# Optimization experiments

Hardware: AMD Instinct MI355X
Metric: run time of the kernel (lower is better)

## Reference

```python
import jax, jax.numpy as jnp
import numpy as np

A_CUBIC = -0.75  # torch grid_sample bicubic convolution coefficient
INTERP_FACTOR = 0.25
WINDOW = 20
STEP = 4


def _cubic_interp_1d(signal):
    # Replicates torch bicubic grid_sample (align_corners=True, border padding)
    # on a (B,1,1,n) tensor, which reduces to 1D cubic convolution (A=-0.75).
    B, n = signal.shape
    num_points = int((n - 1) / INTERP_FACTOR) + 1
    pos = jnp.linspace(0.0, n - 1, num_points)  # sample positions in index space
    i0 = jnp.floor(pos).astype(jnp.int32)
    s = (pos - i0).astype(signal.dtype)  # frac in [0,1)
    A = A_CUBIC
    def w_far(d):   # 1 <= d <= 2
        return ((A * d - 5 * A) * d + 8 * A) * d - 4 * A
    def w_near(d):  # 0 <= d <= 1
        return ((A + 2) * d - (A + 3)) * d * d + 1
    w = jnp.stack([w_far(s + 1), w_near(s), w_near(1 - s), w_far(2 - s)], axis=-1)  # (P,4)
    idx = jnp.clip(i0[:, None] + jnp.arange(-1, 3)[None, :], 0, n - 1)  # border pad, (P,4)
    vals = signal[:, idx]  # (B,P,4)
    return jnp.einsum('bpk,pk->bp', vals, w)


def _apply_kernels(x, gamma_raw):
    # per-row shift so min >= 0 (only if min < 0), then softmax-weighted kernel mix
    m = jnp.min(x, axis=1, keepdims=True)
    x = x - jnp.minimum(m, 0.0)
    gamma = jax.nn.softmax(gamma_raw)
    poly = (x + 1.3) ** 2                      # polynomial: degree=2, offset=1.3
    gauss = jnp.exp(-0.5 * (x - 0.7) ** 2)     # gaussian: center=0.7, sigma=1.0
    return gamma[0] * poly + gamma[1] * gauss


def setup_inputs() -> dict:
    key = jax.random.key(0)
    return {
        'signal': jax.random.normal(key, (4, 1000), dtype=jnp.float32),
        'alpha': jnp.float32(0.15),
        'beta': jnp.float32(0.9),
        'gamma_raw': jnp.array([0.5, 0.5], dtype=jnp.float32),
    }


def reference(signal, alpha, beta, gamma_raw):
    interp = _cubic_interp_1d(signal)              # (B, n)
    ks = _apply_kernels(interp, gamma_raw)         # (B, n)
    B, n = ks.shape
    n_windows = (n - WINDOW) // STEP + 1
    starts = jnp.arange(n_windows) * STEP          # (W,)
    posn = jnp.arange(n)                           # (n,)
    in_win = (posn[None, :] >= starts[:, None]) & (posn[None, :] < starts[:, None] + WINDOW)
    in_win = in_win.astype(ks.dtype)               # (W, n)
    sig = ks[:, None, :]                           # (B,1,n)
    # M: fft of zero-padded window; M1: fft of signal with window zeroed out
    M = jnp.abs(jnp.fft.fft(sig * in_win[None], axis=-1))          # (B,W,n)
    M1 = jnp.abs(jnp.fft.fft(sig * (1.0 - in_win)[None], axis=-1))  # (B,W,n)
    x_max = jnp.max(M, axis=-1, keepdims=True)
    strong = (M > x_max * alpha).astype(M.dtype)
    combined = M1 * M * strong
    result = jnp.minimum(M, combined)              # (B,W,n)
    thr = beta * jnp.max(result.reshape(B, -1), axis=1)[:, None, None]
    result = result * (result > thr).astype(result.dtype)
    return result
```

## Files before the change

### kernel.cpp

```cpp
#include <hip/hip_runtime.h>
#include <math.h>

#define NSIG 1000
#define NP   3997
#define KHALF 1999
#define NW   995
#define WIN  20
#define STEPW 4
#define BATCH 4
#define NCH  125
#define CW   8


__device__ __forceinline__ double interp_at(const float* __restrict__ s, int p) {
    int i0 = p >> 2;
    int si = p & 3;
    double ss = 0.25 * (double)si;
    const double A = -0.75;
    double d0 = ss + 1.0;
    double w0 = ((A * d0 - 5.0 * A) * d0 + 8.0 * A) * d0 - 4.0 * A;
    double w1 = ((A + 2.0) * ss - (A + 3.0)) * ss * ss + 1.0;
    double d2 = 1.0 - ss;
    double w2 = ((A + 2.0) * d2 - (A + 3.0)) * d2 * d2 + 1.0;
    double d3 = 2.0 - ss;
    double w3 = ((A * d3 - 5.0 * A) * d3 + 8.0 * A) * d3 - 4.0 * A;
    int im1 = i0 - 1; if (im1 < 0) im1 = 0;
    int ip1 = i0 + 1; if (ip1 > NSIG - 1) ip1 = NSIG - 1;
    int ip2 = i0 + 2; if (ip2 > NSIG - 1) ip2 = NSIG - 1;
    return w0 * (double)s[im1] + w1 * (double)s[i0] +
           w2 * (double)s[ip1] + w3 * (double)s[ip2];
}

__global__ __launch_bounds__(512) void dft_init_kernel(
        const float* __restrict__ sig, const float* __restrict__ gamma_raw,
        float* __restrict__ ks, float2* __restrict__ tw, float2* __restrict__ S,
        unsigned int* __restrict__ rmax) {
    __shared__ float   lks[NP];
    __shared__ double2 redd[512];
    int b = blockIdx.y;
    int bx = blockIdx.x;
    int tid = threadIdx.x;
    const float* srow = sig + b * NSIG;

    double lmin = 1e300;
    #pragma unroll
    for (int i = 0; i < 8; ++i) {
        int p = tid + i * 512;
        if (p < NP) lmin = fmin(lmin, interp_at(srow, p));
    }
    redd[tid].x = lmin;
    __syncthreads();
    for (int s = 256; s > 0; s >>= 1) {
        if (tid < s) redd[tid].x = fmin(redd[tid].x, redd[tid + s].x);
        __syncthreads();
    }
    double m = fmin(redd[0].x, 0.0);
    double g0r = (double)gamma_raw[0], g1r = (double)gamma_raw[1];
    double mx = fmax(g0r, g1r);
    double e0 = exp(g0r - mx), e1 = exp(g1r - mx);
    double inv = 1.0 / (e0 + e1);
    double g0 = e0 * inv, g1 = e1 * inv;
    #pragma unroll
    for (int i = 0; i < 8; ++i) {
        int p = tid + i * 512;
        if (p < NP) {
            double x = interp_at(srow, p) - m;
            double poly = (x + 1.3) * (x + 1.3);
            double gauss = exp(-0.5 * (x - 0.7) * (x - 0.7));
            float v = (float)(g0 * poly + g1 * gauss);
            lks[p] = v;
            if (bx == 0) ks[b * NP + p] = v;
        }
    }
    if (b == 0 && bx < 8) {
        int mm = bx * 512 + tid;
        if (mm < NP) {
            double ang = -6.283185307179586476925286766559 * ((double)mm / (double)NP);
            double sv, cv; sincos(ang, &sv, &cv);
            tw[mm] = make_float2((float)cv, (float)sv);
        }
        if (bx == 0 && tid < BATCH) rmax[tid] = 0u;
    }
    __syncthreads();

    int kk = tid & 15, tc = tid >> 4;
    int k = bx * 16 + kk;
    double sr = 0.0, si = 0.0;
    if (k < KHALF) {
        int t0 = tc * 125;
        int t1 = t0 + 125; if (t1 > NP) t1 = NP;
        const double TWO_PI = 6.283185307179586476925286766559;
        double base = -TWO_PI / (double)NP;
        double rr, ri;
        sincos(base * (double)k, &ri, &rr);
        int m0 = (k * t0) % NP;
        double pr, pi;
        sincos(base * (double)m0, &pi, &pr);
        for (int t = t0; t < t1; ++t) {
            double kv = (double)lks[t];
            sr = fma(kv, pr, sr);
            si = fma(kv, pi, si);
            double nr = pr * rr - pi * ri;
            double ni = pr * ri + pi * rr;
            pr = nr; pi = ni;
        }
    }
    redd[tid] = make_double2(sr, si);
    __syncthreads();
    for (int s = 256; s >= 16; s >>= 1) {
        if (tid < s) {
            redd[tid].x += redd[tid + s].x;
            redd[tid].y += redd[tid + s].y;
        }
        __syncthreads();
    }
    if (tid < 16) {
        int kw = bx * 16 + tid;
        if (kw < KHALF)
            S[b * NP + kw] = make_float2((float)redd[tid].x, (float)redd[tid].y);
    }
}

__device__ __forceinline__ float wavemax(float x) {
    #pragma unroll
    for (int off = 32; off > 0; off >>= 1)
        x = fmaxf(x, __shfl_xor(x, off));
    return x;
}

#define SLIDE1(n, co, cn) { \
    float ax = fmaf((cn), T##n.x, -(co)); \
    float ay = (cn) * T##n.y; \
    Wx##n = fmaf(ax, Q##n.x, fmaf(-ay, Q##n.y, Wx##n)); \
    Wy##n = fmaf(ax, Q##n.y, fmaf(ay, Q##n.x, Wy##n)); \
    float tq = fmaf(Q##n.x, R##n.x, -(Q##n.y * R##n.y)); \
    Q##n.y = fmaf(Q##n.x, R##n.y, Q##n.y * R##n.x); \
    Q##n.x = tq; }

#define SLIDEJ(co, cn) SLIDE1(0, co, cn) SLIDE1(1, co, cn) SLIDE1(2, co, cn) SLIDE1(3, co, cn)

#define SLIDE4(base) { \
    { float co = kp[(base) + 0], cn = kp[(base) + 20]; SLIDEJ(co, cn) } \
    { float co = kp[(base) + 1], cn = kp[(base) + 21]; SLIDEJ(co, cn) } \
    { float co = kp[(base) + 2], cn = kp[(base) + 22]; SLIDEJ(co, cn) } \
    { float co = kp[(base) + 3], cn = kp[(base) + 23]; SLIDEJ(co, cn) } }

#define WINBODY(w) { \
    float M0 = sqrtf(fmaf(Wx0, Wx0, Wy0 * Wy0)); \
    float M1m = sqrtf(fmaf(Wx1, Wx1, Wy1 * Wy1)); \
    float M2m = sqrtf(fmaf(Wx2, Wx2, Wy2 * Wy2)); \
    float M3m = sqrtf(fmaf(Wx3, Wx3, Wy3 * Wy3)); \
    float lm = fmaxf(fmaxf(M0, M1m), fmaxf(M2m, v3 ? M3m : 0.f)); \
    lm = wavemax(lm); \
    if ((tid & 63) == 0) wred[tid >> 6] = lm; \
    __syncthreads(); \
    float bm = fmaxf(fmaxf(fmaxf(wred[0], wred[1]), fmaxf(wred[2], wred[3])), \
                     fmaxf(fmaxf(wred[4], wred[5]), fmaxf(wred[6], wred[7]))); \
    float cut = bm * alpha; \
    __syncthreads(); \
    if (w0 + (w) < NW) { \
        if (tid == 0) wcut[b * NW + w0 + (w)] = cut; \
        float r0v = 0.f, r1v = 0.f, r2v = 0.f, r3v = 0.f; \
        { float dr = Sv0.x - Wx0, di = Sv0.y - Wy0; float m1 = sqrtf(fmaf(dr, dr, di * di)); \
          if (M0 > cut) r0v = fminf(M0, m1 * M0); } \
        { float dr = Sv1.x - Wx1, di = Sv1.y - Wy1; float m1 = sqrtf(fmaf(dr, dr, di * di)); \
          if (M1m > cut) r1v = fminf(M1m, m1 * M1m); } \
        { float dr = Sv2.x - Wx2, di = Sv2.y - Wy2; float m1 = sqrtf(fmaf(dr, dr, di * di)); \
          if (M2m > cut) r2v = fminf(M2m, m1 * M2m); } \
        { float dr = Sv3.x - Wx3, di = Sv3.y - Wy3; float m1 = sqrtf(fmaf(dr, dr, di * di)); \
          if (M3m > cut) r3v = fminf(M3m, m1 * M3m); } \
        rl = fmaxf(rl, fmaxf(fmaxf(r0v, r1v), fmaxf(r2v, r3v))); \
    } }

__global__ __launch_bounds__(512, 4) void window_kernel(
        const float* __restrict__ ks, const float2* __restrict__ tw,
        const float2* __restrict__ S, const float* __restrict__ alpha_p,
        float* __restrict__ wcut, float* __restrict__ cmax,
        unsigned int* __restrict__ rmax) {
    __shared__ float wred[8];
    int b = blockIdx.y;
    int wc = blockIdx.x;
    int w0 = wc * CW;
    int s0 = w0 * STEPW;
    int tid = threadIdx.x;
    float alpha = *alpha_p;
    const float* kp = ks + b * NP + s0;

    int k0 = tid, k1 = tid + 512, k2 = tid + 1024, k3 = tid + 1536;
    bool v3 = (k3 < KHALF);

    float2 R0 = tw[k0], R1 = tw[k1], R2 = tw[k2], R3 = tw[k3];
    float2 T0 = tw[(20 * k0) % NP], T1 = tw[(20 * k1) % NP],
           T2 = tw[(20 * k2) % NP], T3 = tw[(20 * k3) % NP];
    float2 Q0 = tw[(k0 * s0) % NP], Q1 = tw[(k1 * s0) % NP],
           Q2 = tw[(k2 * s0) % NP], Q3 = tw[(k3 * s0) % NP];
    const float2* Sb = S + b * NP;
    float2 Sv0 = Sb[k0], Sv1 = Sb[k1], Sv2 = Sb[k2], Sv3 = Sb[k3];

    float Dx0 = kp[19], Dy0 = 0.f, Dx1 = kp[19], Dy1 = 0.f,
          Dx2 = kp[19], Dy2 = 0.f, Dx3 = kp[19], Dy3 = 0.f;
    #pragma unroll
    for (int j = 18; j >= 0; --j) {
        float a = kp[j];
        float nx, ny;
        nx = fmaf(Dx0, R0.x, fmaf(-Dy0, R0.y, a));
        ny = fmaf(Dy0, R0.x, Dx0 * R0.y);
        Dx0 = nx; Dy0 = ny;
        nx = fmaf(Dx1, R1.x, fmaf(-Dy1, R1.y, a));
        ny = fmaf(Dy1, R1.x, Dx1 * R1.y);
        Dx1 = nx; Dy1 = ny;
        nx = fmaf(Dx2, R2.x, fmaf(-Dy2, R2.y, a));
        ny = fmaf(Dy2, R2.x, Dx2 * R2.y);
        Dx2 = nx; Dy2 = ny;
        nx = fmaf(Dx3, R3.x, fmaf(-Dy3, R3.y, a));
        ny = fmaf(Dy3, R3.x, Dx3 * R3.y);
        Dx3 = nx; Dy3 = ny;
    }
    float Wx0 = fmaf(Q0.x, Dx0, -(Q0.y * Dy0));
    float Wy0 = fmaf(Q0.x, Dy0, Q0.y * Dx0);
    float Wx1 = fmaf(Q1.x, Dx1, -(Q1.y * Dy1));
    float Wy1 = fmaf(Q1.x, Dy1, Q1.y * Dx1);
    float Wx2 = fmaf(Q2.x, Dx2, -(Q2.y * Dy2));
    float Wy2 = fmaf(Q2.x, Dy2, Q2.y * Dx2);
    float Wx3 = fmaf(Q3.x, Dx3, -(Q3.y * Dy3));
    float Wy3 = fmaf(Q3.x, Dy3, Q3.y * Dx3);

    float rl = 0.f;

    WINBODY(0)
    SLIDE4(0)  WINBODY(1)
    SLIDE4(4)  WINBODY(2)
    SLIDE4(8)  WINBODY(3)
    SLIDE4(12) WINBODY(4)
    SLIDE4(16) WINBODY(5)
    SLIDE4(20) WINBODY(6)
    SLIDE4(24) WINBODY(7)

    rl = wavemax(rl);
    if ((tid & 63) == 0) wred[tid >> 6] = rl;
    __syncthreads();
    if (tid == 0) {
        float bm = fmaxf(fmaxf(fmaxf(wred[0], wred[1]), fmaxf(wred[2], wred[3])),
                         fmaxf(fmaxf(wred[4], wred[5]), fmaxf(wred[6], wred[7])));
        cmax[b * NCH + wc] = bm;
        atomicMax(&rmax[b], __float_as_uint(bm));
    }
}

#define FINBIN(n, kn, valid) { \
    if (valid) { \
        float M = sqrtf(fmaf(Dx##n, Dx##n, Dy##n * Dy##n)); \
        float2 P = tw[((kn) * start) % NP]; \
        float Wr = fmaf(P.x, Dx##n, -(P.y * Dy##n)); \
        float Wi = fmaf(P.x, Dy##n, P.y * Dx##n); \
        float2 Sv = Sb[kn]; \
        float dr = Sv.x - Wr, di = Sv.y - Wi; \
        float M1 = sqrtf(fmaf(dr, dr, di * di)); \
        float res = 0.f; \
        if (M > cut) res = fminf(M, M1 * M); \
        float f = (res > thr) ? res : 0.f; \
        out[base + (kn)] = f; \
        if ((kn) > 0) out[base + NP - (kn)] = f; \
    } }

__global__ __launch_bounds__(512) void finalize_kernel(
        const float* __restrict__ ks, const float2* __restrict__ tw,
        const float2* __restrict__ S, const float* __restrict__ wcut,
        const float* __restrict__ cmax, const unsigned int* __restrict__ rmax,
        const float* __restrict__ beta_p, float* __restrict__ out) {
    int b = blockIdx.y, w = blockIdx.x;
    int tid = threadIdx.x;
    float thr = (*beta_p) * __uint_as_float(rmax[b]);
    size_t base = (size_t)(b * NW + w) * NP;
    if (cmax[b * NCH + (w >> 3)] <= thr) {
        #pragma unroll
        for (int c = 0; c < 8; ++c) {
            int i = tid + c * 512;
            if (i < NP) out[base + i] = 0.f;
        }
        return;
    }
    int start = w * STEPW;
    const float* kp = ks + b * NP + start;
    float cut = wcut[b * NW + w];
    const float2* Sb = S + b * NP;
    int k0 = tid, k1 = tid + 512, k2 = tid + 1024, k3 = tid + 1536;
    bool v3 = (k3 < KHALF);
    float2 R0 = tw[k0], R1 = tw[k1], R2 = tw[k2], R3 = tw[k3];
    float Dx0 = kp[19], Dy0 = 0.f, Dx1 = kp[19], Dy1 = 0.f,
          Dx2 = kp[19], Dy2 = 0.f, Dx3 = kp[19], Dy3 = 0.f;
    #pragma unroll
    for (int j = 18; j >= 0; --j) {
        float a = kp[j];
        float nx, ny;
        nx = fmaf(Dx0, R0.x, fmaf(-Dy0, R0.y, a));
        ny = fmaf(Dy0, R0.x, Dx0 * R0.y);
        Dx0 = nx; Dy0 = ny;
        nx = fmaf(Dx1, R1.x, fmaf(-Dy1, R1.y, a));
        ny = fmaf(Dy1, R1.x, Dx1 * R1.y);
        Dx1 = nx; Dy1 = ny;
        nx = fmaf(Dx2, R2.x, fmaf(-Dy2, R2.y, a));
        ny = fmaf(Dy2, R2.x, Dx2 * R2.y);
        Dx2 = nx; Dy2 = ny;
        nx = fmaf(Dx3, R3.x, fmaf(-Dy3, R3.y, a));
        ny = fmaf(Dy3, R3.x, Dx3 * R3.y);
        Dx3 = nx; Dy3 = ny;
    }
    FINBIN(0, k0, true)
    FINBIN(1, k1, true)
    FINBIN(2, k2, true)
    FINBIN(3, k3, v3)
}

extern "C" void kernel_launch(void* const* d_in, const int* in_sizes, int n_in,
                              void* d_out, int out_size, void* d_ws, size_t ws_size,
                              hipStream_t stream) {
    const float* sig       = (const float*)d_in[0];
    const float* alpha_p   = (const float*)d_in[1];
    const float* beta_p    = (const float*)d_in[2];
    const float* gamma_raw = (const float*)d_in[3];
    char* ws = (char*)d_ws;
    float*        ks   = (float*)(ws + 0);
    float2*       tw   = (float2*)(ws + 65536);
    float2*       S    = (float2*)(ws + 98304);
    unsigned int* rmax = (unsigned int*)(ws + 226304);
    float*        cmax = (float*)(ws + 226432);
    float*        wcut = (float*)(ws + 229376);
    float* out = (float*)d_out;

    hipLaunchKernelGGL(dft_init_kernel, dim3(125, BATCH), dim3(512), 0, stream,
                       sig, gamma_raw, ks, tw, S, rmax);
    hipLaunchKernelGGL(window_kernel,   dim3(NCH, BATCH), dim3(512), 0, stream,
                       ks, tw, S, alpha_p, wcut, cmax, rmax);
    hipLaunchKernelGGL(finalize_kernel, dim3(NW, BATCH),  dim3(512), 0, stream,
                       ks, tw, S, wcut, cmax, rmax, beta_p, out);
}
```

Before: 61.65 us.

## Fuse window and finalize kernels with a software grid barrier

Merges the window-statistics kernel and the finalize kernel into one persistent launch of 500 blocks. A global atomic-counter barrier, reset in the init kernel, separates the max-reduction phase from the output phase. Each block then handles several output rows in a strided loop, and rows that fall below the threshold are zeroed with vectorized float4 stores. This removes one kernel launch and its gap, but it depends on all 500 blocks being co-resident; if they are not, the spin barrier can deadlock.

```diff
diff --git a/kernel.cpp b/kernel.cpp
--- a/kernel.cpp
+++ b/kernel.cpp
@@ -10,6 +10,7 @@
 #define BATCH 4
 #define NCH  125
 #define CW   8
+#define NBLK2 (NCH * BATCH)
 
 
 __device__ __forceinline__ double interp_at(const float* __restrict__ s, int p) {
@@ -34,7 +35,7 @@
 __global__ __launch_bounds__(512) void dft_init_kernel(
         const float* __restrict__ sig, const float* __restrict__ gamma_raw,
         float* __restrict__ ks, float2* __restrict__ tw, float2* __restrict__ S,
-        unsigned int* __restrict__ rmax) {
+        unsigned int* __restrict__ rmax, unsigned int* __restrict__ bar) {
     __shared__ float   lks[NP];
     __shared__ double2 redd[512];
     int b = blockIdx.y;
@@ -80,6 +81,7 @@
             tw[mm] = make_float2((float)cv, (float)sv);
         }
         if (bx == 0 && tid < BATCH) rmax[tid] = 0u;
+        if (bx == 0 && tid == 0) *bar = 0u;
     }
     __syncthreads();
 
@@ -172,81 +174,6 @@
         rl = fmaxf(rl, fmaxf(fmaxf(r0v, r1v), fmaxf(r2v, r3v))); \
     } }
 
-__global__ __launch_bounds__(512, 4) void window_kernel(
-        const float* __restrict__ ks, const float2* __restrict__ tw,
-        const float2* __restrict__ S, const float* __restrict__ alpha_p,
-        float* __restrict__ wcut, float* __restrict__ cmax,
-        unsigned int* __restrict__ rmax) {
-    __shared__ float wred[8];
-    int b = blockIdx.y;
-    int wc = blockIdx.x;
-    int w0 = wc * CW;
-    int s0 = w0 * STEPW;
-    int tid = threadIdx.x;
-    float alpha = *alpha_p;
-    const float* kp = ks + b * NP + s0;
-
-    int k0 = tid, k1 = tid + 512, k2 = tid + 1024, k3 = tid + 1536;
-    bool v3 = (k3 < KHALF);
-
-    float2 R0 = tw[k0], R1 = tw[k1], R2 = tw[k2], R3 = tw[k3];
-    float2 T0 = tw[(20 * k0) % NP], T1 = tw[(20 * k1) % NP],
-           T2 = tw[(20 * k2) % NP], T3 = tw[(20 * k3) % NP];
-    float2 Q0 = tw[(k0 * s0) % NP], Q1 = tw[(k1 * s0) % NP],
-           Q2 = tw[(k2 * s0) % NP], Q3 = tw[(k3 * s0) % NP];
-    const float2* Sb = S + b * NP;
-    float2 Sv0 = Sb[k0], Sv1 = Sb[k1], Sv2 = Sb[k2], Sv3 = Sb[k3];
-
-    float Dx0 = kp[19], Dy0 = 0.f, Dx1 = kp[19], Dy1 = 0.f,
-          Dx2 = kp[19], Dy2 = 0.f, Dx3 = kp[19], Dy3 = 0.f;
-    #pragma unroll
-    for (int j = 18; j >= 0; --j) {
-        float a = kp[j];
-        float nx, ny;
-        nx = fmaf(Dx0, R0.x, fmaf(-Dy0, R0.y, a));
-        ny = fmaf(Dy0, R0.x, Dx0 * R0.y);
-        Dx0 = nx; Dy0 = ny;
-        nx = fmaf(Dx1, R1.x, fmaf(-Dy1, R1.y, a));
-        ny = fmaf(Dy1, R1.x, Dx1 * R1.y);
-        Dx1 = nx; Dy1 = ny;
-        nx = fmaf(Dx2, R2.x, fmaf(-Dy2, R2.y, a));
-        ny = fmaf(Dy2, R2.x, Dx2 * R2.y);
-        Dx2 = nx; Dy2 = ny;
-        nx = fmaf(Dx3, R3.x, fmaf(-Dy3, R3.y, a));
-        ny = fmaf(Dy3, R3.x, Dx3 * R3.y);
-        Dx3 = nx; Dy3 = ny;
-    }
-    float Wx0 = fmaf(Q0.x, Dx0, -(Q0.y * Dy0));
-    float Wy0 = fmaf(Q0.x, Dy0, Q0.y * Dx0);
-    float Wx1 = fmaf(Q1.x, Dx1, -(Q1.y * Dy1));
-    float Wy1 = fmaf(Q1.x, Dy1, Q1.y * Dx1);
-    float Wx2 = fmaf(Q2.x, Dx2, -(Q2.y * Dy2));
-    float Wy2 = fmaf(Q2.x, Dy2, Q2.y * Dx2);
-    float Wx3 = fmaf(Q3.x, Dx3, -(Q3.y * Dy3));
-    float Wy3 = fmaf(Q3.x, Dy3, Q3.y * Dx3);
-
-    float rl = 0.f;
-
-    WINBODY(0)
-    SLIDE4(0)  WINBODY(1)
-    SLIDE4(4)  WINBODY(2)
-    SLIDE4(8)  WINBODY(3)
-    SLIDE4(12) WINBODY(4)
-    SLIDE4(16) WINBODY(5)
-    SLIDE4(20) WINBODY(6)
-    SLIDE4(24) WINBODY(7)
-
-    rl = wavemax(rl);
-    if ((tid & 63) == 0) wred[tid >> 6] = rl;
-    __syncthreads();
-    if (tid == 0) {
-        float bm = fmaxf(fmaxf(fmaxf(wred[0], wred[1]), fmaxf(wred[2], wred[3])),
-                         fmaxf(fmaxf(wred[4], wred[5]), fmaxf(wred[6], wred[7])));
-        cmax[b * NCH + wc] = bm;
-        atomicMax(&rmax[b], __float_as_uint(bm));
-    }
-}
-
 #define FINBIN(n, kn, valid) { \
     if (valid) { \
         float M = sqrtf(fmaf(Dx##n, Dx##n, Dy##n * Dy##n)); \
@@ -263,53 +190,142 @@
         if ((kn) > 0) out[base + NP - (kn)] = f; \
     } }
 
-__global__ __launch_bounds__(512) void finalize_kernel(
+__global__ __launch_bounds__(512, 4) void winfin_kernel(
         const float* __restrict__ ks, const float2* __restrict__ tw,
-        const float2* __restrict__ S, const float* __restrict__ wcut,
-        const float* __restrict__ cmax, const unsigned int* __restrict__ rmax,
-        const float* __restrict__ beta_p, float* __restrict__ out) {
-    int b = blockIdx.y, w = blockIdx.x;
+        const float2* __restrict__ S, const float* __restrict__ alpha_p,
+        const float* __restrict__ beta_p, float* __restrict__ wcut,
+        float* __restrict__ cmax, unsigned int* __restrict__ rmax,
+        unsigned int* __restrict__ bar, float* __restrict__ out) {
+    __shared__ float wred[8];
+    int bid = blockIdx.x;
+    int b = bid & 3;
+    int wc = bid >> 2;
+    int w0 = wc * CW;
+    int s0 = w0 * STEPW;
     int tid = threadIdx.x;
-    float thr = (*beta_p) * __uint_as_float(rmax[b]);
-    size_t base = (size_t)(b * NW + w) * NP;
-    if (cmax[b * NCH + (w >> 3)] <= thr) {
-        #pragma unroll
-        for (int c = 0; c < 8; ++c) {
-            int i = tid + c * 512;
-            if (i < NP) out[base + i] = 0.f;
-        }
-        return;
-    }
-    int start = w * STEPW;
-    const float* kp = ks + b * NP + start;
-    float cut = wcut[b * NW + w];
-    const float2* Sb = S + b * NP;
+    float alpha = *alpha_p;
+    const float* kp = ks + b * NP + s0;
+
     int k0 = tid, k1 = tid + 512, k2 = tid + 1024, k3 = tid + 1536;
     bool v3 = (k3 < KHALF);
-    float2 R0 = tw[k0], R1 = tw[k1], R2 = tw[k2], R3 = tw[k3];
-    float Dx0 = kp[19], Dy0 = 0.f, Dx1 = kp[19], Dy1 = 0.f,
-          Dx2 = kp[19], Dy2 = 0.f, Dx3 = kp[19], Dy3 = 0.f;
-    #pragma unroll
-    for (int j = 18; j >= 0; --j) {
-        float a = kp[j];
-        float nx, ny;
-        nx = fmaf(Dx0, R0.x, fmaf(-Dy0, R0.y, a));
-        ny = fmaf(Dy0, R0.x, Dx0 * R0.y);
-        Dx0 = nx; Dy0 = ny;
-        nx = fmaf(Dx1, R1.x, fmaf(-Dy1, R1.y, a));
-        ny = fmaf(Dy1, R1.x, Dx1 * R1.y);
-        Dx1 = nx; Dy1 = ny;
-        nx = fmaf(Dx2, R2.x, fmaf(-Dy2, R2.y, a));
-        ny = fmaf(Dy2, R2.x, Dx2 * R2.y);
-        Dx2 = nx; Dy2 = ny;
-        nx = fmaf(Dx3, R3.x, fmaf(-Dy3, R3.y, a));
-        ny = fmaf(Dy3, R3.x, Dx3 * R3.y);
-        Dx3 = nx; Dy3 = ny;
-    }
-    FINBIN(0, k0, true)
-    FINBIN(1, k1, true)
-    FINBIN(2, k2, true)
-    FINBIN(3, k3, v3)
+
+    {
+        float2 R0 = tw[k0], R1 = tw[k1], R2 = tw[k2], R3 = tw[k3];
+        float2 T0 = tw[(20 * k0) % NP], T1 = tw[(20 * k1) % NP],
+               T2 = tw[(20 * k2) % NP], T3 = tw[(20 * k3) % NP];
+        float2 Q0 = tw[(k0 * s0) % NP], Q1 = tw[(k1 * s0) % NP],
+               Q2 = tw[(k2 * s0) % NP], Q3 = tw[(k3 * s0) % NP];
+        const float2* Sb = S + b * NP;
+        float2 Sv0 = Sb[k0], Sv1 = Sb[k1], Sv2 = Sb[k2], Sv3 = Sb[k3];
+
+        float Dx0 = kp[19], Dy0 = 0.f, Dx1 = kp[19], Dy1 = 0.f,
+              Dx2 = kp[19], Dy2 = 0.f, Dx3 = kp[19], Dy3 = 0.f;
+        #pragma unroll
+        for (int j = 18; j >= 0; --j) {
+            float a = kp[j];
+            float nx, ny;
+            nx = fmaf(Dx0, R0.x, fmaf(-Dy0, R0.y, a));
+            ny = fmaf(Dy0, R0.x, Dx0 * R0.y);
+            Dx0 = nx; Dy0 = ny;
+            nx = fmaf(Dx1, R1.x, fmaf(-Dy1, R1.y, a));
+            ny = fmaf(Dy1, R1.x, Dx1 * R1.y);
+            Dx1 = nx; Dy1 = ny;
+            nx = fmaf(Dx2, R2.x, fmaf(-Dy2, R2.y, a));
+            ny = fmaf(Dy2, R2.x, Dx2 * R2.y);
+            Dx2 = nx; Dy2 = ny;
+            nx = fmaf(Dx3, R3.x, fmaf(-Dy3, R3.y, a));
+            ny = fmaf(Dy3, R3.x, Dx3 * R3.y);
+            Dx3 = nx; Dy3 = ny;
+        }
+        float Wx0 = fmaf(Q0.x, Dx0, -(Q0.y * Dy0));
+        float Wy0 = fmaf(Q0.x, Dy0, Q0.y * Dx0);
+        float Wx1 = fmaf(Q1.x, Dx1, -(Q1.y * Dy1));
+        float Wy1 = fmaf(Q1.x, Dy1, Q1.y * Dx1);
+        float Wx2 = fmaf(Q2.x, Dx2, -(Q2.y * Dy2));
+        float Wy2 = fmaf(Q2.x, Dy2, Q2.y * Dx2);
+        float Wx3 = fmaf(Q3.x, Dx3, -(Q3.y * Dy3));
+        float Wy3 = fmaf(Q3.x, Dy3, Q3.y * Dx3);
+
+        float rl = 0.f;
+
+        WINBODY(0)
+        SLIDE4(0)  WINBODY(1)
+        SLIDE4(4)  WINBODY(2)
+        SLIDE4(8)  WINBODY(3)
+        SLIDE4(12) WINBODY(4)
+        SLIDE4(16) WINBODY(5)
+        SLIDE4(20) WINBODY(6)
+        SLIDE4(24) WINBODY(7)
+
+        rl = wavemax(rl);
+        if ((tid & 63) == 0) wred[tid >> 6] = rl;
+        __syncthreads();
+        if (tid == 0) {
+            float bm = fmaxf(fmaxf(fmaxf(wred[0], wred[1]), fmaxf(wred[2], wred[3])),
+                             fmaxf(fmaxf(wred[4], wred[5]), fmaxf(wred[6], wred[7])));
+            cmax[b * NCH + wc] = bm;
+            atomicMax(&rmax[b], __float_as_uint(bm));
+        }
+    }
+
+    __syncthreads();
+    __threadfence();
+    if (tid == 0) {
+        atomicAdd(bar, 1u);
+        while (atomicAdd(bar, 0u) < (unsigned)NBLK2)
+            __builtin_amdgcn_s_sleep(2);
+    }
+    __syncthreads();
+    __threadfence();
+
+    float beta = *beta_p;
+    for (int i = 0; i < 8; ++i) {
+        int rr = bid + i * NBLK2;
+        if (rr >= BATCH * NW) break;
+        int fb = rr / NW;
+        int w = rr - fb * NW;
+        float thr = beta * __uint_as_float(rmax[fb]);
+        size_t base = (size_t)rr * NP;
+        if (cmax[fb * NCH + (w >> 3)] <= thr) {
+            int h = (4 - (int)(base & 3)) & 3;
+            int nv = (NP - h) >> 2;
+            int t0 = h + (nv << 2);
+            float4* vp = (float4*)(out + base + h);
+            float4 z4 = make_float4(0.f, 0.f, 0.f, 0.f);
+            for (int v = tid; v < nv; v += 512) vp[v] = z4;
+            if (tid < h) out[base + tid] = 0.f;
+            if (tid < NP - t0) out[base + t0 + tid] = 0.f;
+            continue;
+        }
+        int start = w * STEPW;
+        const float* kpf = ks + fb * NP + start;
+        float cut = wcut[fb * NW + w];
+        const float2* Sb = S + fb * NP;
+        float2 R0 = tw[k0], R1 = tw[k1], R2 = tw[k2], R3 = tw[k3];
+        float Dx0 = kpf[19], Dy0 = 0.f, Dx1 = kpf[19], Dy1 = 0.f,
+              Dx2 = kpf[19], Dy2 = 0.f, Dx3 = kpf[19], Dy3 = 0.f;
+        #pragma unroll
+        for (int j = 18; j >= 0; --j) {
+            float a = kpf[j];
+            float nx, ny;
+            nx = fmaf(Dx0, R0.x, fmaf(-Dy0, R0.y, a));
+            ny = fmaf(Dy0, R0.x, Dx0 * R0.y);
+            Dx0 = nx; Dy0 = ny;
+            nx = fmaf(Dx1, R1.x, fmaf(-Dy1, R1.y, a));
+            ny = fmaf(Dy1, R1.x, Dx1 * R1.y);
+            Dx1 = nx; Dy1 = ny;
+            nx = fmaf(Dx2, R2.x, fmaf(-Dy2, R2.y, a));
+            ny = fmaf(Dy2, R2.x, Dx2 * R2.y);
+            Dx2 = nx; Dy2 = ny;
+            nx = fmaf(Dx3, R3.x, fmaf(-Dy3, R3.y, a));
+            ny = fmaf(Dy3, R3.x, Dx3 * R3.y);
+            Dx3 = nx; Dy3 = ny;
+        }
+        FINBIN(0, k0, true)
+        FINBIN(1, k1, true)
+        FINBIN(2, k2, true)
+        FINBIN(3, k3, v3)
+    }
 }
 
 extern "C" void kernel_launch(void* const* d_in, const int* in_sizes, int n_in,
@@ -324,14 +340,13 @@
     float2*       tw   = (float2*)(ws + 65536);
     float2*       S    = (float2*)(ws + 98304);
     unsigned int* rmax = (unsigned int*)(ws + 226304);
+    unsigned int* bar  = (unsigned int*)(ws + 226320);
     float*        cmax = (float*)(ws + 226432);
     float*        wcut = (float*)(ws + 229376);
     float* out = (float*)d_out;
 
     hipLaunchKernelGGL(dft_init_kernel, dim3(125, BATCH), dim3(512), 0, stream,
-                       sig, gamma_raw, ks, tw, S, rmax);
-    hipLaunchKernelGGL(window_kernel,   dim3(NCH, BATCH), dim3(512), 0, stream,
-                       ks, tw, S, alpha_p, wcut, cmax, rmax);
-    hipLaunchKernelGGL(finalize_kernel, dim3(NW, BATCH),  dim3(512), 0, stream,
-                       ks, tw, S, wcut, cmax, rmax, beta_p, out);
-}
+                       sig, gamma_raw, ks, tw, S, rmax, bar);
+    hipLaunchKernelGGL(winfin_kernel,   dim3(NBLK2),      dim3(512), 0, stream,
+                       ks, tw, S, alpha_p, beta_p, wcut, cmax, rmax, bar, out);
+}
```

Result: slower. 199.8 us (+224.1%).
